# Kernel optimization log

Hardware: AMD Instinct MI355X
Metric: run time of the kernel (lower is better)

## Reference

```python
import jax, jax.numpy as jnp
import numpy as np

H = 12  # num_attention_heads


def setup_inputs() -> dict:
    key = jax.random.key(0)
    ks = jax.random.split(key, 16)
    B, S, D = 8, 768, 768
    sc = 0.02
    return {
        "hidden_states": jax.random.normal(ks[0], (B, S, D), jnp.float32),
        "instruction_context": jax.random.normal(ks[1], (B, S, D), jnp.float32),
        "Wq": jax.random.normal(ks[2], (D, D), jnp.float32) * sc,
        "bq": jnp.zeros((D,), jnp.float32),
        "Wk": jax.random.normal(ks[3], (D, D), jnp.float32) * sc,
        "bk": jnp.zeros((D,), jnp.float32),
        "Wv": jax.random.normal(ks[4], (D, D), jnp.float32) * sc,
        "bv": jnp.zeros((D,), jnp.float32),
        "Wcs": jax.random.normal(ks[5], (D, H), jnp.float32) * sc,
        "bcs": jnp.zeros((H,), jnp.float32),
        "Wg": jax.random.normal(ks[6], (D, H), jnp.float32) * sc,
        "bg": jnp.zeros((H,), jnp.float32),
        "Wa": jax.random.normal(ks[7], (D, D), jnp.float32) * sc,
        "ba": jnp.zeros((D,), jnp.float32),
    }


def reference(hidden_states, instruction_context, Wq, bq, Wk, bk, Wv, bv,
              Wcs, bcs, Wg, bg, Wa, ba):
    B, S, D = hidden_states.shape
    dh = D // H
    split = lambda x: x.reshape(B, S, H, dh).transpose(0, 2, 1, 3)  # [B,H,S,dh]
    q = split(hidden_states @ Wq + bq)
    k = split(hidden_states @ Wk + bk)
    v = split(hidden_states @ Wv + bv)

    scores = jnp.einsum("bhqd,bhkd->bhqk", q, k) / jnp.sqrt(jnp.float32(dh))

    # code-structure additive bias: per (head, query), broadcast over keys
    code_structure = hidden_states @ Wcs + bcs            # [B,S,H]
    scores = scores + code_structure.transpose(0, 2, 1)[..., None]

    # syntax-aware sigmoid gate: per (head, query), broadcast over keys
    gate = jax.nn.sigmoid(hidden_states @ Wg + bg)        # [B,S,H]
    scores = scores * gate.transpose(0, 2, 1)[..., None]

    # alignment bias: projection over hidden dim acts as key-dim bias (S == D)
    align = instruction_context @ Wa + ba                 # [B,S,D] with D==S
    scores = scores + align[:, None, :, :]

    probs = jax.nn.softmax(scores, axis=-1)               # [B,H,S,S]
    ctx = jnp.einsum("bhqk,bhkd->bhqd", probs, v)
    ctx = ctx.transpose(0, 2, 1, 3).reshape(B, S, D)
    return ctx, probs
```

## Files before the change

### kernel.cpp

```cpp
#include <hip/hip_runtime.h>
#include <stdint.h>
#include <math.h>

typedef __attribute__((ext_vector_type(8))) short short8b;
typedef __attribute__((ext_vector_type(4))) float f32x4;
typedef __attribute__((ext_vector_type(8))) unsigned short u16x8;
typedef __attribute__((ext_vector_type(4))) unsigned int u32x4;

#define S 768
#define DD 768
#define H 12
#define DH 64

static __device__ __forceinline__ unsigned short f2bf(float f) {
  union { float f; unsigned u; } v; v.f = f;
  unsigned u = v.u;
  u += 0x7FFFu + ((u >> 16) & 1u);
  return (unsigned short)(u >> 16);
}

static __device__ __forceinline__ void gload_lds16(const void* g, void* l) {
  __builtin_amdgcn_global_load_lds((const __attribute__((address_space(1))) void*)g,
                                   (__attribute__((address_space(3))) void*)l, 16, 0, 0);
}

__global__ __launch_bounds__(256) void prep_kernel(
    const float* __restrict__ HS, const float* __restrict__ IC,
    const float* __restrict__ W0, const float* __restrict__ W1,
    const float* __restrict__ W2, const float* __restrict__ W3,
    unsigned short* __restrict__ HSb, unsigned short* __restrict__ ICb,
    unsigned short* __restrict__ T0, unsigned short* __restrict__ T1,
    unsigned short* __restrict__ T2, unsigned short* __restrict__ T3, int n8) {
  __shared__ float t[32][33];
  int id = blockIdx.x;
  int tid = threadIdx.x;
  if (id < 4608) {
    int i = id * 256 + tid;
    const float* in; unsigned short* out;
    if (i >= n8) { in = IC; out = ICb; i -= n8; }
    else         { in = HS; out = HSb; }
    const float4* p = (const float4*)in;
    float4 a = p[2*(size_t)i], b = p[2*(size_t)i + 1];
    u16x8 o;
    o[0] = f2bf(a.x); o[1] = f2bf(a.y); o[2] = f2bf(a.z); o[3] = f2bf(a.w);
    o[4] = f2bf(b.x); o[5] = f2bf(b.y); o[6] = f2bf(b.z); o[7] = f2bf(b.w);
    *(u16x8*)(out + 8*(size_t)i) = o;
    return;
  }
  int wid = id - 4608;
  int z = wid / 576;
  int r = wid % 576;
  int k0 = (r % 24) * 32, n0 = (r / 24) * 32;
  const float* W = (z == 0) ? W0 : (z == 1) ? W1 : (z == 2) ? W2 : W3;
  unsigned short* T = (z == 0) ? T0 : (z == 1) ? T1 : (z == 2) ? T2 : T3;
  int tx = tid & 31, ty = tid >> 5;
#pragma unroll
  for (int i = 0; i < 4; i++)
    t[ty + i*8][tx] = W[(size_t)(k0 + ty + i*8) * DD + n0 + tx];
  __syncthreads();
#pragma unroll
  for (int i = 0; i < 4; i++)
    T[(size_t)(n0 + ty + i*8) * DD + k0 + tx] = f2bf(t[tx][ty + i*8]);
}

__global__ __launch_bounds__(256) void gate_kernel(const float* __restrict__ HS,
                                                   const float* __restrict__ Wg,
                                                   const float* __restrict__ bg,
                                                   float* __restrict__ gate) {
  __shared__ float wgt[H][DD];
  int tid = threadIdx.x;
  for (int i = tid; i < DD*H; i += 256) {
    int d = i / H, h = i % H;
    wgt[h][d] = Wg[i];
  }
  __syncthreads();
  int w = tid >> 6, lane = tid & 63;
  int row0 = blockIdx.x * 16 + w * 4;
  for (int r = 0; r < 4; r++) {
    int row = row0 + r;
    const float* hrow = HS + (size_t)row * DD;
    float hv[12];
#pragma unroll
    for (int i = 0; i < 12; i++) hv[i] = hrow[lane + i*64];
    float acc[H];
#pragma unroll
    for (int h = 0; h < H; h++) {
      float s = 0.f;
#pragma unroll
      for (int i = 0; i < 12; i++) s += hv[i] * wgt[h][lane + i*64];
      acc[h] = s;
    }
#pragma unroll
    for (int m = 1; m < 64; m <<= 1) {
#pragma unroll
      for (int h = 0; h < H; h++) acc[h] += __shfl_xor(acc[h], m);
    }
    if (lane < H) {
      float v = 0.f;
#pragma unroll
      for (int h = 0; h < H; h++) v = (lane == h) ? acc[h] : v;
      v += bg[lane];
      gate[(size_t)row * H + lane] = 1.f / (1.f + __expf(-v));
    }
  }
}

__global__ __launch_bounds__(256) void gemm4_kernel(
    const unsigned short* __restrict__ HSb, const unsigned short* __restrict__ ICb,
    const unsigned short* __restrict__ WqT, const unsigned short* __restrict__ WkT,
    const unsigned short* __restrict__ WvT, const unsigned short* __restrict__ WaT,
    const float* __restrict__ bq, const float* __restrict__ bk,
    const float* __restrict__ bv, const float* __restrict__ ba,
    unsigned short* __restrict__ Qb, unsigned short* __restrict__ Kb,
    unsigned short* __restrict__ Vt, float* __restrict__ alignf) {
  int id = blockIdx.x;
  int wid = (id & 7) * 144 + (id >> 3);
  int z = wid / 288;
  int rr = wid % 288;
  int bx = rr / 6, by = rr % 6;
  int m0 = bx * 128, n0 = by * 128;

  const unsigned short* A  = (z == 3) ? ICb : HSb;
  const unsigned short* BT = (z == 0) ? WqT : (z == 1) ? WkT : (z == 2) ? WvT : WaT;
  const float* bias = (z == 0) ? bq : (z == 1) ? bk : (z == 2) ? bv : ba;
  unsigned short* Cb = (z == 0) ? Qb : (z == 1) ? Kb : (unsigned short*)0;

  __shared__ __align__(16) char smem[65536];

  int tid = threadIdx.x;
  int w = tid >> 6, lane = tid & 63;
  int cl = lane & 15, g = lane >> 4;
  int wm = (w & 1) * 64, wn = (w >> 1) * 64;

  f32x4 acc[4][4];
#pragma unroll
  for (int r = 0; r < 4; r++)
#pragma unroll
    for (int c = 0; c < 4; c++) acc[r][c] = (f32x4){0.f, 0.f, 0.f, 0.f};

  int srow = (lane >> 3) + w * 8;
  int slot = lane & 7;

  auto stage = [&](int buf, int ks) {
    char* ad = smem + buf * 32768;
    char* bd = ad + 16384;
#pragma unroll
    for (int i = 0; i < 4; i++) {
      int row = i*32 + srow;
      gload_lds16(A  + (size_t)(m0 + row)*DD + ks + slot*8, ad + i*4096 + w*1024);
      gload_lds16(BT + (size_t)(n0 + row)*DD + ks + slot*8, bd + i*4096 + w*1024);
    }
  };

  stage(0, 0);
  __syncthreads();
  for (int t = 0; t < 12; ++t) {
    int cur = t & 1;
    if (t + 1 < 12) stage(cur ^ 1, (t + 1) * 64);
    const char* As = smem + cur * 32768;
    const char* Bs = As + 16384;
#pragma unroll
    for (int kk = 0; kk < 2; kk++) {
      short8b af[4], bf[4];
#pragma unroll
      for (int r = 0; r < 4; r++) {
        int row = wm + r*16 + cl;
        af[r] = *(const short8b*)(As + row*128 + kk*64 + g*16);
      }
#pragma unroll
      for (int c = 0; c < 4; c++) {
        int row = wn + c*16 + cl;
        bf[c] = *(const short8b*)(Bs + row*128 + kk*64 + g*16);
      }
#pragma unroll
      for (int r = 0; r < 4; r++)
#pragma unroll
        for (int c = 0; c < 4; c++)
          acc[r][c] = __builtin_amdgcn_mfma_f32_16x16x32_bf16(af[r], bf[c], acc[r][c], 0, 0, 0);
    }
    __syncthreads();
  }

  if (z <= 1) {
#pragma unroll
    for (int c = 0; c < 4; c++) {
      int col = wn + c*16 + cl;
      float bvv = bias[n0 + col];
#pragma unroll
      for (int r = 0; r < 4; r++) {
#pragma unroll
        for (int q = 0; q < 4; q++) {
          int row = wm + r*16 + g*4 + q;
          int byte = (row*256 + col*2) ^ ((row & 7) << 4);
          *(unsigned short*)(smem + byte) = f2bf(acc[r][c][q] + bvv);
        }
      }
    }
    __syncthreads();
#pragma unroll
    for (int it = 0; it < 8; it++) {
      int idx = it*256 + tid;
      int row = idx >> 4, ch = idx & 15;
      u32x4 v = *(const u32x4*)(smem + ((row*256 + ch*16) ^ ((row & 7) << 4)));
      *(u32x4*)(Cb + (size_t)(m0 + row)*DD + n0 + ch*8) = v;
    }
  } else if (z == 2) {
#pragma unroll
    for (int c = 0; c < 4; c++) {
      int col = wn + c*16 + cl;
      float bvv = bias[n0 + col];
#pragma unroll
      for (int r = 0; r < 4; r++) {
#pragma unroll
        for (int q = 0; q < 4; q++) {
          int row = wm + r*16 + g*4 + q;
          int byte = (col*256 + row*2) ^ ((col & 7) << 4);
          *(unsigned short*)(smem + byte) = f2bf(acc[r][c][q] + bvv);
        }
      }
    }
    __syncthreads();
    int b = m0 / S, s0 = m0 % S;
#pragma unroll
    for (int it = 0; it < 8; it++) {
      int idx = it*256 + tid;
      int row = idx >> 4, ch = idx & 15;
      u32x4 v = *(const u32x4*)(smem + ((row*256 + ch*16) ^ ((row & 7) << 4)));
      *(u32x4*)(Vt + (size_t)(b*DD + n0 + row)*S + s0 + ch*8) = v;
    }
  } else {
#pragma unroll
    for (int half = 0; half < 2; half++) {
      if ((w & 1) == half) {
#pragma unroll
        for (int c = 0; c < 4; c++) {
          int col = wn + c*16 + cl;
          float bvv = bias[n0 + col];
#pragma unroll
          for (int r = 0; r < 4; r++) {
#pragma unroll
            for (int q = 0; q < 4; q++) {
              int rl = r*16 + g*4 + q;
              int byte = (rl*512 + col*4) ^ ((rl & 7) << 4);
              *(float*)(smem + byte) = acc[r][c][q] + bvv;
            }
          }
        }
      }
      __syncthreads();
#pragma unroll
      for (int it = 0; it < 8; it++) {
        int idx = it*256 + tid;
        int row = idx >> 5, ch = idx & 31;
        u32x4 v = *(const u32x4*)(smem + ((row*512 + ch*16) ^ ((row & 7) << 4)));
        *(u32x4*)(alignf + (size_t)(m0 + half*64 + row)*DD + n0 + ch*4) = v;
      }
      __syncthreads();
    }
  }
}

__global__ __launch_bounds__(256) void attn_kernel(const unsigned short* __restrict__ Qb,
                                                   const unsigned short* __restrict__ Kb,
                                                   const unsigned short* __restrict__ Vt,
                                                   const float* __restrict__ alignf,
                                                   const float* __restrict__ gate,
                                                   float* __restrict__ ctx,
                                                   float* __restrict__ probs) {
  __shared__ __align__(16) char smemA[16384];
  __shared__ __align__(16) unsigned short Ps[2][32*64];
  __shared__ float smx[4][16], ssm[4][16];

  int tid = threadIdx.x;
  int w = tid >> 6, lane = tid & 63;
  int cl = lane & 15, g = lane >> 4;
  int id = blockIdx.x;
  int b = id & 7, t = id >> 3;
  int h = t % H, q0 = (t / H) * 32;
  int bh = b * H + h;
  int trow = (w >> 1) * 16;
  int tc0 = (w & 1) * 2;

  short8b qf[2];
  {
    const unsigned short* qp = Qb + (size_t)(b*S + q0 + trow + cl)*DD + h*DH + g*8;
    qf[0] = *(const short8b*)qp;
    qf[1] = *(const short8b*)(qp + 32);
  }
  f32x4 g4v;
#pragma unroll
  for (int r = 0; r < 4; r++)
    g4v[r] = gate[(size_t)(b*S + q0 + trow + g*4 + r)*H + h] * 0.125f;

  const unsigned short* kbase = Kb + (size_t)b*S*DD + h*DH;
  const unsigned short* vbase = Vt + (size_t)bh*DH*S;
  const float* abase = alignf + (size_t)(b*S + q0 + trow + g*4)*S;

  int srow = (lane >> 3) + w * 8;
  int slot = lane & 7;
  auto stageK = [&](int buf, int k0) {
    char* dst = smemA + buf * 8192;
#pragma unroll
    for (int i = 0; i < 2; i++) {
      int row = i*32 + srow;
      gload_lds16(kbase + (size_t)(k0 + row)*DD + slot*8, dst + i*4096 + w*1024);
    }
  };

  f32x4 vs0[12], vs1[12];
  stageK(0, 0);
  __syncthreads();
#pragma unroll
  for (int c = 0; c < 12; c++) {
    int k0 = c * 64;
    if (c + 1 < 12) stageK((c + 1) & 1, k0 + 64);
    const char* Ks = smemA + (c & 1) * 8192;
    f32x4 sc0 = (f32x4){0.f,0.f,0.f,0.f}, sc1 = (f32x4){0.f,0.f,0.f,0.f};
#pragma unroll
    for (int kk = 0; kk < 2; kk++) {
      int r0 = tc0*16 + cl;
      sc0 = __builtin_amdgcn_mfma_f32_16x16x32_bf16(qf[kk], *(const short8b*)(Ks + r0*128 + kk*64 + g*16), sc0, 0, 0, 0);
      sc1 = __builtin_amdgcn_mfma_f32_16x16x32_bf16(qf[kk], *(const short8b*)(Ks + (r0+16)*128 + kk*64 + g*16), sc1, 0, 0, 0);
    }
    f32x4 a0, a1;
#pragma unroll
    for (int r = 0; r < 4; r++) {
      a0[r] = abase[(size_t)r*S + k0 + tc0*16 + cl];
      a1[r] = abase[(size_t)r*S + k0 + tc0*16 + 16 + cl];
    }
    vs0[c] = sc0 * g4v + a0;
    vs1[c] = sc1 * g4v + a1;
    __syncthreads();
  }

  float m[4], ssr[4];
#pragma unroll
  for (int r = 0; r < 4; r++) {
    float mm = -INFINITY;
#pragma unroll
    for (int c = 0; c < 12; c++)
      mm = fmaxf(mm, fmaxf(vs0[c][r], vs1[c][r]));
    mm = fmaxf(mm, __shfl_xor(mm, 1));
    mm = fmaxf(mm, __shfl_xor(mm, 2));
    mm = fmaxf(mm, __shfl_xor(mm, 4));
    mm = fmaxf(mm, __shfl_xor(mm, 8));
    m[r] = mm;
  }
  if (cl == 0) {
#pragma unroll
    for (int r = 0; r < 4; r++) smx[w][g*4 + r] = m[r];
  }
  __syncthreads();
#pragma unroll
  for (int r = 0; r < 4; r++) m[r] = fmaxf(m[r], smx[w ^ 1][g*4 + r]);
  float sum[4];
#pragma unroll
  for (int r = 0; r < 4; r++) {
    float s = 0.f;
#pragma unroll
    for (int c = 0; c < 12; c++) {
      float e0 = __expf(vs0[c][r] - m[r]);
      float e1 = __expf(vs1[c][r] - m[r]);
      vs0[c][r] = e0;
      vs1[c][r] = e1;
      s += e0 + e1;
    }
    s += __shfl_xor(s, 1);
    s += __shfl_xor(s, 2);
    s += __shfl_xor(s, 4);
    s += __shfl_xor(s, 8);
    sum[r] = s;
  }
  if (cl == 0) {
#pragma unroll
    for (int r = 0; r < 4; r++) ssm[w][g*4 + r] = sum[r];
  }
  __syncthreads();
#pragma unroll
  for (int r = 0; r < 4; r++) ssr[r] = 1.f / (sum[r] + ssm[w ^ 1][g*4 + r]);

  f32x4 oc0 = (f32x4){0.f,0.f,0.f,0.f}, oc1 = (f32x4){0.f,0.f,0.f,0.f};
#pragma unroll
  for (int tt = 0; tt < 6; tt++) {
#pragma unroll
    for (int i = 0; i < 4; i++) {
      int u = i*256 + tid;
      int row = u >> 4, sl = u & 15;
      gload_lds16(vbase + (size_t)row*S + tt*128 + sl*8, smemA + i*4096 + w*1024);
    }
#pragma unroll
    for (int j = 0; j < 2; j++) {
      int c = tt*2 + j;
#pragma unroll
      for (int r = 0; r < 4; r++) {
        int ql = trow + g*4 + r;
        float p0 = vs0[c][r] * ssr[r];
        float p1 = vs1[c][r] * ssr[r];
        int off0 = (ql*128 + (tc0*16 + cl)*2) ^ ((ql & 7) << 4);
        int off1 = (ql*128 + (tc0*16 + 16 + cl)*2) ^ ((ql & 7) << 4);
        *(unsigned short*)((char*)Ps[j] + off0) = f2bf(p0);
        *(unsigned short*)((char*)Ps[j] + off1) = f2bf(p1);
      }
    }
    __syncthreads();
#pragma unroll
    for (int j = 0; j < 2; j++) {
      int c = tt*2 + j;
      int k0 = c * 64;
#pragma unroll
      for (int r = 0; r < 4; r++) {
        int ql = trow + g*4 + r;
        float* pr = probs + ((size_t)bh*S + q0 + ql)*S + k0;
        __builtin_nontemporal_store(vs0[c][r] * ssr[r], pr + tc0*16 + cl);
        __builtin_nontemporal_store(vs1[c][r] * ssr[r], pr + tc0*16 + 16 + cl);
      }
#pragma unroll
      for (int kk = 0; kk < 2; kk++) {
        int prow = trow + cl;
        int po = (prow*128 + kk*64 + g*16) ^ ((prow & 7) << 4);
        short8b pf = *(const short8b*)((const char*)Ps[j] + po);
        int d0 = tc0*16 + cl;
        oc0 = __builtin_amdgcn_mfma_f32_16x16x32_bf16(pf, *(const short8b*)(smemA + d0*256 + j*128 + kk*64 + g*16), oc0, 0, 0, 0);
        oc1 = __builtin_amdgcn_mfma_f32_16x16x32_bf16(pf, *(const short8b*)(smemA + (d0+16)*256 + j*128 + kk*64 + g*16), oc1, 0, 0, 0);
      }
    }
    __syncthreads();
  }

  float* ctxs = (float*)smemA;
#pragma unroll
  for (int r = 0; r < 4; r++) {
    int ql = trow + g*4 + r;
    ctxs[ql*68 + tc0*16 + cl]      = oc0[r];
    ctxs[ql*68 + tc0*16 + 16 + cl] = oc1[r];
  }
  __syncthreads();
#pragma unroll
  for (int j = 0; j < 2; j++) {
    int idx = tid + j*256;
    int row = idx >> 4, c4 = idx & 15;
    f32x4 v = *(const f32x4*)(ctxs + row*68 + c4*4);
    __builtin_nontemporal_store(v, (f32x4*)(ctx + (size_t)(b*S + q0 + row)*DD + h*DH + c4*4));
  }
}

extern "C" void kernel_launch(void* const* d_in, const int* in_sizes, int n_in,
                              void* d_out, int out_size, void* d_ws, size_t ws_size,
                              hipStream_t stream) {
  const float* HS = (const float*)d_in[0];
  const float* IC = (const float*)d_in[1];
  const float* Wq = (const float*)d_in[2];
  const float* bq = (const float*)d_in[3];
  const float* Wk = (const float*)d_in[4];
  const float* bk = (const float*)d_in[5];
  const float* Wv = (const float*)d_in[6];
  const float* bv = (const float*)d_in[7];
  const float* Wg = (const float*)d_in[10];
  const float* bg = (const float*)d_in[11];
  const float* Wa = (const float*)d_in[12];
  const float* ba = (const float*)d_in[13];

  float* ctx   = (float*)d_out;
  float* probs = ctx + (size_t)8 * S * DD;

  char* ws = (char*)d_ws;
  size_t off = 0;
  auto alloc = [&](size_t n) { char* p = ws + off; off += (n + 255) & ~(size_t)255; return p; };
  unsigned short* HSb = (unsigned short*)alloc(9437184);
  unsigned short* ICb = (unsigned short*)alloc(9437184);
  unsigned short* WqT = (unsigned short*)alloc(1179648);
  unsigned short* WkT = (unsigned short*)alloc(1179648);
  unsigned short* WvT = (unsigned short*)alloc(1179648);
  unsigned short* WaT = (unsigned short*)alloc(1179648);
  unsigned short* Qb  = (unsigned short*)alloc(9437184);
  unsigned short* Kb  = (unsigned short*)alloc(9437184);
  unsigned short* Vt  = (unsigned short*)alloc(9437184);
  float* alignf = (float*)alloc(18874368);
  float* gatep  = (float*)alloc(294912);

  int n8 = 8 * S * DD / 8;
  prep_kernel<<<dim3(6912), dim3(256), 0, stream>>>(HS, IC, Wq, Wk, Wv, Wa,
                                                    HSb, ICb, WqT, WkT, WvT, WaT, n8);
  gemm4_kernel<<<dim3(1152), dim3(256), 0, stream>>>(HSb, ICb, WqT, WkT, WvT, WaT,
                                                     bq, bk, bv, ba, Qb, Kb, Vt, alignf);
  gate_kernel<<<dim3(384), dim3(256), 0, stream>>>(HS, Wg, bg, gatep);
  attn_kernel<<<dim3(2304), dim3(256), 0, stream>>>(Qb, Kb, Vt, alignf, gatep, ctx, probs);
}
```

Measured before the change: 153.3 us.

## Store alignment bias as bf16 and fold gate computation into prep kernel

The alignment projection output is now written as bf16 through the same swizzled LDS epilogue as Q/K, and the attention kernel reads and widens it. This halves the alignment buffer traffic in both the GEMM epilogue and the attention kernel. The gate kernel's work is merged into the prep launch as extra blocks, removing one kernel launch. In exchange, align values lose precision, and every prep block now reserves the large gate weight shared buffer, which may reduce occupancy of the conversion blocks.

```diff
diff --git a/kernel.cpp b/kernel.cpp
--- a/kernel.cpp
+++ b/kernel.cpp
@@ -18,6 +18,9 @@
   u += 0x7FFFu + ((u >> 16) & 1u);
   return (unsigned short)(u >> 16);
 }
+static __device__ __forceinline__ float bf2f(unsigned short u) {
+  union { unsigned u; float f; } v; v.u = (unsigned)u << 16; return v.f;
+}
 
 static __device__ __forceinline__ void gload_lds16(const void* g, void* l) {
   __builtin_amdgcn_global_load_lds((const __attribute__((address_space(1))) void*)g,
@@ -28,10 +31,12 @@
     const float* __restrict__ HS, const float* __restrict__ IC,
     const float* __restrict__ W0, const float* __restrict__ W1,
     const float* __restrict__ W2, const float* __restrict__ W3,
+    const float* __restrict__ Wg, const float* __restrict__ bg,
     unsigned short* __restrict__ HSb, unsigned short* __restrict__ ICb,
     unsigned short* __restrict__ T0, unsigned short* __restrict__ T1,
-    unsigned short* __restrict__ T2, unsigned short* __restrict__ T3, int n8) {
-  __shared__ float t[32][33];
+    unsigned short* __restrict__ T2, unsigned short* __restrict__ T3,
+    float* __restrict__ gate, int n8) {
+  __shared__ __align__(16) float shm[H*DD];
   int id = blockIdx.x;
   int tid = threadIdx.x;
   if (id < 4608) {
@@ -47,35 +52,32 @@
     *(u16x8*)(out + 8*(size_t)i) = o;
     return;
   }
-  int wid = id - 4608;
-  int z = wid / 576;
-  int r = wid % 576;
-  int k0 = (r % 24) * 32, n0 = (r / 24) * 32;
-  const float* W = (z == 0) ? W0 : (z == 1) ? W1 : (z == 2) ? W2 : W3;
-  unsigned short* T = (z == 0) ? T0 : (z == 1) ? T1 : (z == 2) ? T2 : T3;
-  int tx = tid & 31, ty = tid >> 5;
-#pragma unroll
-  for (int i = 0; i < 4; i++)
-    t[ty + i*8][tx] = W[(size_t)(k0 + ty + i*8) * DD + n0 + tx];
-  __syncthreads();
-#pragma unroll
-  for (int i = 0; i < 4; i++)
-    T[(size_t)(n0 + ty + i*8) * DD + k0 + tx] = f2bf(t[tx][ty + i*8]);
-}
-
-__global__ __launch_bounds__(256) void gate_kernel(const float* __restrict__ HS,
-                                                   const float* __restrict__ Wg,
-                                                   const float* __restrict__ bg,
-                                                   float* __restrict__ gate) {
-  __shared__ float wgt[H][DD];
-  int tid = threadIdx.x;
+  if (id < 6912) {
+    int wid = id - 4608;
+    int z = wid / 576;
+    int r = wid % 576;
+    int k0 = (r % 24) * 32, n0 = (r / 24) * 32;
+    const float* W = (z == 0) ? W0 : (z == 1) ? W1 : (z == 2) ? W2 : W3;
+    unsigned short* T = (z == 0) ? T0 : (z == 1) ? T1 : (z == 2) ? T2 : T3;
+    float (*t)[33] = (float(*)[33])shm;
+    int tx = tid & 31, ty = tid >> 5;
+#pragma unroll
+    for (int i = 0; i < 4; i++)
+      t[ty + i*8][tx] = W[(size_t)(k0 + ty + i*8) * DD + n0 + tx];
+    __syncthreads();
+#pragma unroll
+    for (int i = 0; i < 4; i++)
+      T[(size_t)(n0 + ty + i*8) * DD + k0 + tx] = f2bf(t[tx][ty + i*8]);
+    return;
+  }
+  float (*wgt)[DD] = (float(*)[DD])shm;
   for (int i = tid; i < DD*H; i += 256) {
     int d = i / H, h = i % H;
     wgt[h][d] = Wg[i];
   }
   __syncthreads();
   int w = tid >> 6, lane = tid & 63;
-  int row0 = blockIdx.x * 16 + w * 4;
+  int row0 = (id - 6912) * 16 + w * 4;
   for (int r = 0; r < 4; r++) {
     int row = row0 + r;
     const float* hrow = HS + (size_t)row * DD;
@@ -112,7 +114,7 @@
     const float* __restrict__ bq, const float* __restrict__ bk,
     const float* __restrict__ bv, const float* __restrict__ ba,
     unsigned short* __restrict__ Qb, unsigned short* __restrict__ Kb,
-    unsigned short* __restrict__ Vt, float* __restrict__ alignf) {
+    unsigned short* __restrict__ Vt, unsigned short* __restrict__ alignb) {
   int id = blockIdx.x;
   int wid = (id & 7) * 144 + (id >> 3);
   int z = wid / 288;
@@ -123,7 +125,7 @@
   const unsigned short* A  = (z == 3) ? ICb : HSb;
   const unsigned short* BT = (z == 0) ? WqT : (z == 1) ? WkT : (z == 2) ? WvT : WaT;
   const float* bias = (z == 0) ? bq : (z == 1) ? bk : (z == 2) ? bv : ba;
-  unsigned short* Cb = (z == 0) ? Qb : (z == 1) ? Kb : (unsigned short*)0;
+  unsigned short* Cb = (z == 0) ? Qb : (z == 1) ? Kb : (z == 3) ? alignb : (unsigned short*)0;
 
   __shared__ __align__(16) char smem[65536];
 
@@ -181,7 +183,8 @@
     __syncthreads();
   }
 
-  if (z <= 1) {
+  __syncthreads();
+  if (z != 2) {
 #pragma unroll
     for (int c = 0; c < 4; c++) {
       int col = wn + c*16 + cl;
@@ -204,7 +207,7 @@
       u32x4 v = *(const u32x4*)(smem + ((row*256 + ch*16) ^ ((row & 7) << 4)));
       *(u32x4*)(Cb + (size_t)(m0 + row)*DD + n0 + ch*8) = v;
     }
-  } else if (z == 2) {
+  } else {
 #pragma unroll
     for (int c = 0; c < 4; c++) {
       int col = wn + c*16 + cl;
@@ -228,42 +231,13 @@
       u32x4 v = *(const u32x4*)(smem + ((row*256 + ch*16) ^ ((row & 7) << 4)));
       *(u32x4*)(Vt + (size_t)(b*DD + n0 + row)*S + s0 + ch*8) = v;
     }
-  } else {
-#pragma unroll
-    for (int half = 0; half < 2; half++) {
-      if ((w & 1) == half) {
-#pragma unroll
-        for (int c = 0; c < 4; c++) {
-          int col = wn + c*16 + cl;
-          float bvv = bias[n0 + col];
-#pragma unroll
-          for (int r = 0; r < 4; r++) {
-#pragma unroll
-            for (int q = 0; q < 4; q++) {
-              int rl = r*16 + g*4 + q;
-              int byte = (rl*512 + col*4) ^ ((rl & 7) << 4);
-              *(float*)(smem + byte) = acc[r][c][q] + bvv;
-            }
-          }
-        }
-      }
-      __syncthreads();
-#pragma unroll
-      for (int it = 0; it < 8; it++) {
-        int idx = it*256 + tid;
-        int row = idx >> 5, ch = idx & 31;
-        u32x4 v = *(const u32x4*)(smem + ((row*512 + ch*16) ^ ((row & 7) << 4)));
-        *(u32x4*)(alignf + (size_t)(m0 + half*64 + row)*DD + n0 + ch*4) = v;
-      }
-      __syncthreads();
-    }
   }
 }
 
 __global__ __launch_bounds__(256) void attn_kernel(const unsigned short* __restrict__ Qb,
                                                    const unsigned short* __restrict__ Kb,
                                                    const unsigned short* __restrict__ Vt,
-                                                   const float* __restrict__ alignf,
+                                                   const unsigned short* __restrict__ alignb,
                                                    const float* __restrict__ gate,
                                                    float* __restrict__ ctx,
                                                    float* __restrict__ probs) {
@@ -294,7 +268,7 @@
 
   const unsigned short* kbase = Kb + (size_t)b*S*DD + h*DH;
   const unsigned short* vbase = Vt + (size_t)bh*DH*S;
-  const float* abase = alignf + (size_t)(b*S + q0 + trow + g*4)*S;
+  const unsigned short* abase = alignb + (size_t)(b*S + q0 + trow + g*4)*S;
 
   int srow = (lane >> 3) + w * 8;
   int slot = lane & 7;
@@ -325,8 +299,8 @@
     f32x4 a0, a1;
 #pragma unroll
     for (int r = 0; r < 4; r++) {
-      a0[r] = abase[(size_t)r*S + k0 + tc0*16 + cl];
-      a1[r] = abase[(size_t)r*S + k0 + tc0*16 + 16 + cl];
+      a0[r] = bf2f(abase[(size_t)r*S + k0 + tc0*16 + cl]);
+      a1[r] = bf2f(abase[(size_t)r*S + k0 + tc0*16 + 16 + cl]);
     }
     vs0[c] = sc0 * g4v + a0;
     vs1[c] = sc1 * g4v + a1;
@@ -475,14 +449,13 @@
   unsigned short* Qb  = (unsigned short*)alloc(9437184);
   unsigned short* Kb  = (unsigned short*)alloc(9437184);
   unsigned short* Vt  = (unsigned short*)alloc(9437184);
-  float* alignf = (float*)alloc(18874368);
+  unsigned short* alignb = (unsigned short*)alloc(9437184);
   float* gatep  = (float*)alloc(294912);
 
   int n8 = 8 * S * DD / 8;
-  prep_kernel<<<dim3(6912), dim3(256), 0, stream>>>(HS, IC, Wq, Wk, Wv, Wa,
-                                                    HSb, ICb, WqT, WkT, WvT, WaT, n8);
+  prep_kernel<<<dim3(7296), dim3(256), 0, stream>>>(HS, IC, Wq, Wk, Wv, Wa, Wg, bg,
+                                                    HSb, ICb, WqT, WkT, WvT, WaT, gatep, n8);
   gemm4_kernel<<<dim3(1152), dim3(256), 0, stream>>>(HSb, ICb, WqT, WkT, WvT, WaT,
-                                                     bq, bk, bv, ba, Qb, Kb, Vt, alignf);
-  gate_kernel<<<dim3(384), dim3(256), 0, stream>>>(HS, Wg, bg, gatep);
-  attn_kernel<<<dim3(2304), dim3(256), 0, stream>>>(Qb, Kb, Vt, alignf, gatep, ctx, probs);
-}
+                                                     bq, bk, bv, ba, Qb, Kb, Vt, alignb);
+  attn_kernel<<<dim3(2304), dim3(256), 0, stream>>>(Qb, Kb, Vt, alignb, gatep, ctx, probs);
+}
```

New measurement: 187.6 us. +22.4%, slower.

## Halve attention query tile and split keys across waves with LDS reduction

Applied to the files above, without the earlier changes.

The attention kernel now handles 16 query rows per block instead of 32, doubling the grid. Each of the four waves takes a 16-key slice of every 64-key chunk. Softmax max and sum are reduced across all four waves through shared memory, and each wave computes a partial P·V over its key slice. The partial contexts are summed pairwise through LDS before the store. This roughly halves per-thread register state and adds parallelism, at the cost of reloading K and V tiles twice as often per query and an extra cross-wave reduction step.

```diff
diff --git a/kernel.cpp b/kernel.cpp
--- a/kernel.cpp
+++ b/kernel.cpp
@@ -268,7 +268,7 @@
                                                    float* __restrict__ ctx,
                                                    float* __restrict__ probs) {
   __shared__ __align__(16) char smemA[16384];
-  __shared__ __align__(16) unsigned short Ps[2][32*64];
+  __shared__ __align__(16) char Psm[4*1280];
   __shared__ float smx[4][16], ssm[4][16];
 
   int tid = threadIdx.x;
@@ -276,25 +276,23 @@
   int cl = lane & 15, g = lane >> 4;
   int id = blockIdx.x;
   int b = id & 7, t = id >> 3;
-  int h = t % H, q0 = (t / H) * 32;
+  int h = t % H, q0 = (t / H) * 16;
   int bh = b * H + h;
-  int trow = (w >> 1) * 16;
-  int tc0 = (w & 1) * 2;
 
   short8b qf[2];
   {
-    const unsigned short* qp = Qb + (size_t)(b*S + q0 + trow + cl)*DD + h*DH + g*8;
+    const unsigned short* qp = Qb + (size_t)(b*S + q0 + cl)*DD + h*DH + g*8;
     qf[0] = *(const short8b*)qp;
     qf[1] = *(const short8b*)(qp + 32);
   }
   f32x4 g4v;
 #pragma unroll
   for (int r = 0; r < 4; r++)
-    g4v[r] = gate[(size_t)(b*S + q0 + trow + g*4 + r)*H + h] * 0.125f;
+    g4v[r] = gate[(size_t)(b*S + q0 + g*4 + r)*H + h] * 0.125f;
 
   const unsigned short* kbase = Kb + (size_t)b*S*DD + h*DH;
   const unsigned short* vbase = Vt + (size_t)bh*DH*S;
-  const float* abase = alignf + (size_t)(b*S + q0 + trow + g*4)*S;
+  const float* abase = alignf + (size_t)(b*S + q0 + g*4)*S;
 
   int srow = (lane >> 3) + w * 8;
   int slot = lane & 7;
@@ -307,7 +305,7 @@
     }
   };
 
-  f32x4 vs0[12], vs1[12];
+  f32x4 vs[12];
   stageK(0, 0);
   __syncthreads();
 #pragma unroll
@@ -315,21 +313,15 @@
     int k0 = c * 64;
     if (c + 1 < 12) stageK((c + 1) & 1, k0 + 64);
     const char* Ks = smemA + (c & 1) * 8192;
-    f32x4 sc0 = (f32x4){0.f,0.f,0.f,0.f}, sc1 = (f32x4){0.f,0.f,0.f,0.f};
-#pragma unroll
-    for (int kk = 0; kk < 2; kk++) {
-      int r0 = tc0*16 + cl;
-      sc0 = __builtin_amdgcn_mfma_f32_16x16x32_bf16(qf[kk], *(const short8b*)(Ks + r0*128 + kk*64 + g*16), sc0, 0, 0, 0);
-      sc1 = __builtin_amdgcn_mfma_f32_16x16x32_bf16(qf[kk], *(const short8b*)(Ks + (r0+16)*128 + kk*64 + g*16), sc1, 0, 0, 0);
-    }
-    f32x4 a0, a1;
-#pragma unroll
-    for (int r = 0; r < 4; r++) {
-      a0[r] = abase[(size_t)r*S + k0 + tc0*16 + cl];
-      a1[r] = abase[(size_t)r*S + k0 + tc0*16 + 16 + cl];
-    }
-    vs0[c] = sc0 * g4v + a0;
-    vs1[c] = sc1 * g4v + a1;
+    int r0 = w*16 + cl;
+    f32x4 sc = (f32x4){0.f,0.f,0.f,0.f};
+    sc = __builtin_amdgcn_mfma_f32_16x16x32_bf16(qf[0], *(const short8b*)(Ks + r0*128 + g*16), sc, 0, 0, 0);
+    sc = __builtin_amdgcn_mfma_f32_16x16x32_bf16(qf[1], *(const short8b*)(Ks + r0*128 + 64 + g*16), sc, 0, 0, 0);
+    f32x4 a;
+#pragma unroll
+    for (int r = 0; r < 4; r++)
+      a[r] = abase[(size_t)r*S + k0 + w*16 + cl];
+    vs[c] = sc * g4v + a;
     __syncthreads();
   }
 
@@ -338,8 +330,7 @@
   for (int r = 0; r < 4; r++) {
     float mm = -INFINITY;
 #pragma unroll
-    for (int c = 0; c < 12; c++)
-      mm = fmaxf(mm, fmaxf(vs0[c][r], vs1[c][r]));
+    for (int c = 0; c < 12; c++) mm = fmaxf(mm, vs[c][r]);
     mm = fmaxf(mm, __shfl_xor(mm, 1));
     mm = fmaxf(mm, __shfl_xor(mm, 2));
     mm = fmaxf(mm, __shfl_xor(mm, 4));
@@ -352,18 +343,18 @@
   }
   __syncthreads();
 #pragma unroll
-  for (int r = 0; r < 4; r++) m[r] = fmaxf(m[r], smx[w ^ 1][g*4 + r]);
+  for (int r = 0; r < 4; r++)
+    m[r] = fmaxf(fmaxf(smx[0][g*4 + r], smx[1][g*4 + r]),
+                 fmaxf(smx[2][g*4 + r], smx[3][g*4 + r]));
   float sum[4];
 #pragma unroll
   for (int r = 0; r < 4; r++) {
     float s = 0.f;
 #pragma unroll
     for (int c = 0; c < 12; c++) {
-      float e0 = __expf(vs0[c][r] - m[r]);
-      float e1 = __expf(vs1[c][r] - m[r]);
-      vs0[c][r] = e0;
-      vs1[c][r] = e1;
-      s += e0 + e1;
+      float e = __expf(vs[c][r] - m[r]);
+      vs[c][r] = e;
+      s += e;
     }
     s += __shfl_xor(s, 1);
     s += __shfl_xor(s, 2);
@@ -377,9 +368,13 @@
   }
   __syncthreads();
 #pragma unroll
-  for (int r = 0; r < 4; r++) ssr[r] = 1.f / (sum[r] + ssm[w ^ 1][g*4 + r]);
-
-  f32x4 oc0 = (f32x4){0.f,0.f,0.f,0.f}, oc1 = (f32x4){0.f,0.f,0.f,0.f};
+  for (int r = 0; r < 4; r++)
+    ssr[r] = 1.f / (ssm[0][g*4 + r] + ssm[1][g*4 + r] + ssm[2][g*4 + r] + ssm[3][g*4 + r]);
+
+  char* Pw = Psm + w * 1280;
+  f32x4 oc[4];
+#pragma unroll
+  for (int dt = 0; dt < 4; dt++) oc[dt] = (f32x4){0.f,0.f,0.f,0.f};
 #pragma unroll
   for (int tt = 0; tt < 6; tt++) {
 #pragma unroll
@@ -393,54 +388,64 @@
       int c = tt*2 + j;
 #pragma unroll
       for (int r = 0; r < 4; r++) {
-        int ql = trow + g*4 + r;
-        float p0 = vs0[c][r] * ssr[r];
-        float p1 = vs1[c][r] * ssr[r];
-        int off0 = (ql*128 + (tc0*16 + cl)*2) ^ ((ql & 7) << 4);
-        int off1 = (ql*128 + (tc0*16 + 16 + cl)*2) ^ ((ql & 7) << 4);
-        *(unsigned short*)((char*)Ps[j] + off0) = f2bf(p0);
-        *(unsigned short*)((char*)Ps[j] + off1) = f2bf(p1);
+        int q = g*4 + r;
+        *(unsigned short*)(Pw + q*80 + j*32 + cl*2) = f2bf(vs[c][r] * ssr[r]);
       }
     }
     __syncthreads();
 #pragma unroll
     for (int j = 0; j < 2; j++) {
       int c = tt*2 + j;
-      int k0 = c * 64;
 #pragma unroll
       for (int r = 0; r < 4; r++) {
-        int ql = trow + g*4 + r;
-        float* pr = probs + ((size_t)bh*S + q0 + ql)*S + k0;
-        __builtin_nontemporal_store(vs0[c][r] * ssr[r], pr + tc0*16 + cl);
-        __builtin_nontemporal_store(vs1[c][r] * ssr[r], pr + tc0*16 + 16 + cl);
-      }
-#pragma unroll
-      for (int kk = 0; kk < 2; kk++) {
-        int prow = trow + cl;
-        int po = (prow*128 + kk*64 + g*16) ^ ((prow & 7) << 4);
-        short8b pf = *(const short8b*)((const char*)Ps[j] + po);
-        int d0 = tc0*16 + cl;
-        oc0 = __builtin_amdgcn_mfma_f32_16x16x32_bf16(pf, *(const short8b*)(smemA + d0*256 + j*128 + kk*64 + g*16), oc0, 0, 0, 0);
-        oc1 = __builtin_amdgcn_mfma_f32_16x16x32_bf16(pf, *(const short8b*)(smemA + (d0+16)*256 + j*128 + kk*64 + g*16), oc1, 0, 0, 0);
-      }
-    }
-    __syncthreads();
-  }
-
-  float* ctxs = (float*)smemA;
-#pragma unroll
-  for (int r = 0; r < 4; r++) {
-    int ql = trow + g*4 + r;
-    ctxs[ql*68 + tc0*16 + cl]      = oc0[r];
-    ctxs[ql*68 + tc0*16 + 16 + cl] = oc1[r];
-  }
-  __syncthreads();
-#pragma unroll
-  for (int j = 0; j < 2; j++) {
-    int idx = tid + j*256;
-    int row = idx >> 4, c4 = idx & 15;
-    f32x4 v = *(const f32x4*)(ctxs + row*68 + c4*4);
-    __builtin_nontemporal_store(v, (f32x4*)(ctx + (size_t)(b*S + q0 + row)*DD + h*DH + c4*4));
+        float* pr = probs + ((size_t)bh*S + q0 + g*4 + r)*S + c*64;
+        __builtin_nontemporal_store(vs[c][r] * ssr[r], pr + w*16 + cl);
+      }
+    }
+    {
+      short8b pf = *(const short8b*)(Pw + cl*80 + g*16);
+      int scol = ((g >> 1)*64 + w*16 + (g & 1)*8) * 2;
+#pragma unroll
+      for (int dt = 0; dt < 4; dt++) {
+        const short8b vf = *(const short8b*)(smemA + (dt*16 + cl)*256 + scol);
+        oc[dt] = __builtin_amdgcn_mfma_f32_16x16x32_bf16(pf, vf, oc[dt], 0, 0, 0);
+      }
+    }
+    __syncthreads();
+  }
+
+  float* cA = (float*)smemA;
+  float* cB = (float*)(smemA + 4352);
+  if (w == 0) {
+#pragma unroll
+    for (int dt = 0; dt < 4; dt++)
+#pragma unroll
+      for (int r = 0; r < 4; r++) cA[(g*4 + r)*68 + dt*16 + cl] = oc[dt][r];
+  } else if (w == 2) {
+#pragma unroll
+    for (int dt = 0; dt < 4; dt++)
+#pragma unroll
+      for (int r = 0; r < 4; r++) cB[(g*4 + r)*68 + dt*16 + cl] = oc[dt][r];
+  }
+  __syncthreads();
+  if (w == 1) {
+#pragma unroll
+    for (int dt = 0; dt < 4; dt++)
+#pragma unroll
+      for (int r = 0; r < 4; r++) cA[(g*4 + r)*68 + dt*16 + cl] += oc[dt][r];
+  } else if (w == 3) {
+#pragma unroll
+    for (int dt = 0; dt < 4; dt++)
+#pragma unroll
+      for (int r = 0; r < 4; r++) cB[(g*4 + r)*68 + dt*16 + cl] += oc[dt][r];
+  }
+  __syncthreads();
+  {
+    int row = tid >> 4, d4 = (tid & 15) * 4;
+    f32x4 va = *(const f32x4*)(cA + row*68 + d4);
+    f32x4 vb = *(const f32x4*)(cB + row*68 + d4);
+    __builtin_nontemporal_store(va + vb,
+        (f32x4*)(ctx + (size_t)(b*S + q0 + row)*DD + h*DH + d4));
   }
 }
 
@@ -484,5 +489,5 @@
   gemm4_kernel<<<dim3(1152), dim3(256), 0, stream>>>(HSb, ICb, WqT, WkT, WvT, WaT,
                                                      bq, bk, bv, ba, Qb, Kb, Vt, alignf);
   gate_kernel<<<dim3(384), dim3(256), 0, stream>>>(HS, Wg, bg, gatep);
-  attn_kernel<<<dim3(2304), dim3(256), 0, stream>>>(Qb, Kb, Vt, alignf, gatep, ctx, probs);
-}
+  attn_kernel<<<dim3(4608), dim3(256), 0, stream>>>(Qb, Kb, Vt, alignf, gatep, ctx, probs);
+}
```

Measured after the change: 162.3 us. 5.9% more time.
